# Kernel tuning notes

Hardware: AMD Instinct MI355X
Metric: run time of the kernel (lower is better)

## Reference

```python
import jax, jax.numpy as jnp
import numpy as np

NUM_HEADS = 8
NUM_LAYERS = 4
BASE_THR = 0.5     # AdaptiveLIF base_threshold (state reset -> no adaptation on single step)
TAU_MEM = 5.0      # tau_mem (single step from zero state: mem = decay*0 + x = x)
SURR_SLOPE = 5.0   # fast-sigmoid surrogate slope (forward path unaffected)
EPS = 1e-5
NEG = -1e9


@jax.custom_vjp
def spike(u):
    return (u > 0.0).astype(u.dtype)

def _spike_fwd(u):
    return (u > 0.0).astype(u.dtype), u

def _spike_bwd(u, g):
    return (g / (1.0 + SURR_SLOPE * jnp.abs(u)) ** 2,)

spike.defvjp(_spike_fwd, _spike_bwd)


def lif(x):
    # AdaptiveLIF, single timestep from reset state: mem = x, thr = base_threshold
    return spike(x - BASE_THR)


def layer_norm(x, g, b):
    m = jnp.mean(x, axis=-1, keepdims=True)
    v = jnp.mean((x - m) ** 2, axis=-1, keepdims=True)
    return (x - m) * jax.lax.rsqrt(v + EPS) * g + b


def dsa(x, wq, bq, wk, bk, wv, bv, wo, bo, top_k):
    # Dynamic Sparse Attention: dense scores -> per-query top-k mask -> softmax -> AV
    B, T, D = x.shape
    H = NUM_HEADS
    dh = D // H

    def heads(w, bias):
        return (x @ w.T + bias).reshape(B, T, H, dh).transpose(0, 2, 1, 3)  # [B,H,T,dh]

    q, k, v = heads(wq, bq), heads(wk, bk), heads(wv, bv)
    scores = jnp.einsum('bhqd,bhkd->bhqk', q, k) / jnp.sqrt(jnp.asarray(dh, x.dtype))
    vals, idx = jax.lax.top_k(scores, top_k)  # [B,H,T,K]

    # scatter top-k values into a -inf-filled score matrix (exact top-k sparsity)
    N = B * H * T
    rows = jnp.arange(N)[:, None]
    sp = jnp.full((N, T), NEG, scores.dtype).at[rows, idx.reshape(N, top_k)].set(vals.reshape(N, top_k))
    attn = jax.nn.softmax(sp.reshape(B, H, T, T), axis=-1)

    out = jnp.einsum('bhqk,bhkd->bhqd', attn, v)
    out = out.transpose(0, 2, 1, 3).reshape(B, T, D)
    out = out @ wo.T + bo
    return lif(out)  # spiking output of attention


def ffn(x, w1, b1, w2, b2):
    h = lif(x @ w1.T + b1)
    return lif(h @ w2.T + b2)


def setup_inputs() -> dict:
    key = jax.random.key(0)
    ks = jax.random.split(key, 16)
    L, D, F, IN, OUT, B, T = NUM_LAYERS, 512, 2048, 128, 256, 2, 2048
    s = 0.02
    return {
        'x': jax.random.normal(ks[0], (B, T, IN), jnp.float32),
        'emb_w': jax.random.normal(ks[1], (D, IN), jnp.float32) * s,
        'emb_b': jnp.zeros((D,), jnp.float32),
        'pos_emb': jax.random.normal(ks[2], (1, T, D), jnp.float32) * s,
        'wq': jax.random.normal(ks[3], (L, D, D), jnp.float32) * s,
        'bq': jnp.zeros((L, D), jnp.float32),
        'wk': jax.random.normal(ks[4], (L, D, D), jnp.float32) * s,
        'bk': jnp.zeros((L, D), jnp.float32),
        'wv': jax.random.normal(ks[5], (L, D, D), jnp.float32) * s,
        'bv': jnp.zeros((L, D), jnp.float32),
        'wo': jax.random.normal(ks[6], (L, D, D), jnp.float32) * s,
        'bo': jnp.zeros((L, D), jnp.float32),
        'ln1_g': jnp.ones((L, D), jnp.float32),
        'ln1_b': jnp.zeros((L, D), jnp.float32),
        'fc1_w': jax.random.normal(ks[7], (L, F, D), jnp.float32) * s,
        'fc1_b': jnp.zeros((L, F), jnp.float32),
        'fc2_w': jax.random.normal(ks[8], (L, D, F), jnp.float32) * s,
        'fc2_b': jnp.zeros((L, D), jnp.float32),
        'ln2_g': jnp.ones((L, D), jnp.float32),
        'ln2_b': jnp.zeros((L, D), jnp.float32),
        'fnorm_g': jnp.ones((D,), jnp.float32),
        'fnorm_b': jnp.zeros((D,), jnp.float32),
        'cls_w': jax.random.normal(ks[9], (OUT, D), jnp.float32) * s,
        'cls_b': jnp.zeros((OUT,), jnp.float32),
        'top_k': 32,
    }


def reference(x, emb_w, emb_b, pos_emb, wq, bq, wk, bk, wv, bv, wo, bo,
              ln1_g, ln1_b, fc1_w, fc1_b, fc2_w, fc2_b, ln2_g, ln2_b,
              fnorm_g, fnorm_b, cls_w, cls_b, top_k):
    B, T, _ = x.shape
    h = x @ emb_w.T + emb_b + pos_emb[:, :T, :]
    for l in range(NUM_LAYERS):
        a = dsa(h, wq[l], bq[l], wk[l], bk[l], wv[l], bv[l], wo[l], bo[l], top_k)
        h = layer_norm(h + a, ln1_g[l], ln1_b[l])
        f = ffn(h, fc1_w[l], fc1_b[l], fc2_w[l], fc2_b[l])
        h = layer_norm(h + f, ln2_g[l], ln2_b[l])
    h = layer_norm(h, fnorm_g, fnorm_b)
    pooled = jnp.mean(h, axis=1)  # [B, D]
    return pooled @ cls_w.T + cls_b
```

## Files before the change

kernel.cpp:

```cpp
#include <hip/hip_runtime.h>
#include <math.h>
#include <float.h>

#define T_SEQ  2048
#define DMODEL 512
#define NHEAD  8
#define DHEAD  64
#define FDIM   2048
#define NLAYER 4
#define NB     2
#define MROWS  (NB*T_SEQ)

typedef _Float16 f16x8 __attribute__((ext_vector_type(8)));
typedef float    f32x4 __attribute__((ext_vector_type(4)));

__device__ __forceinline__ void async16(const _Float16* g, _Float16* l) {
    __builtin_amdgcn_global_load_lds(
        (const __attribute__((address_space(1))) unsigned int*)g,
        (__attribute__((address_space(3))) unsigned int*)l, 16, 0, 0);
}

template<int BN, int EPI>
__global__ __launch_bounds__(256) void gemm_k(
    const float* __restrict__ A, const float* __restrict__ W,
    const float* __restrict__ bias, const float* __restrict__ pos,
    float* __restrict__ C, int M, int N, int K)
{
    constexpr int BM = 128;
    constexpr int BK = 32;
    constexpr int MN = BN / 16;
    __shared__ float As[BK][BM + 4];
    __shared__ float Ws[BK][BN + 4];
    const int tid = threadIdx.x;
    const int n0 = blockIdx.x * BN;
    const int m0 = blockIdx.y * BM;
    const int tx = tid & 15;
    const int ty = tid >> 4;

    float acc[8][MN];
    #pragma unroll
    for (int i = 0; i < 8; ++i)
        #pragma unroll
        for (int j = 0; j < MN; ++j) acc[i][j] = 0.f;

    for (int k0 = 0; k0 < K; k0 += BK) {
        #pragma unroll
        for (int it = 0; it < 4; ++it) {
            int qq = tid + 256 * it;
            int m = qq >> 3, kq = qq & 7;
            float4 v4 = *(const float4*)(A + (size_t)(m0 + m) * K + k0 + kq * 4);
            As[kq*4+0][m] = v4.x; As[kq*4+1][m] = v4.y;
            As[kq*4+2][m] = v4.z; As[kq*4+3][m] = v4.w;
        }
        #pragma unroll
        for (int it = 0; it < BN/32; ++it) {
            int qq = tid + 256 * it;
            int n = qq >> 3, kq = qq & 7;
            float4 v4 = *(const float4*)(W + (size_t)(n0 + n) * K + k0 + kq * 4);
            Ws[kq*4+0][n] = v4.x; Ws[kq*4+1][n] = v4.y;
            Ws[kq*4+2][n] = v4.z; Ws[kq*4+3][n] = v4.w;
        }
        __syncthreads();
        for (int kk = 0; kk < BK; ++kk) {
            float a[8], b[MN];
            float4 a0 = *(const float4*)&As[kk][ty*8];
            float4 a1 = *(const float4*)&As[kk][ty*8+4];
            a[0]=a0.x; a[1]=a0.y; a[2]=a0.z; a[3]=a0.w;
            a[4]=a1.x; a[5]=a1.y; a[6]=a1.z; a[7]=a1.w;
            float4 b0 = *(const float4*)&Ws[kk][tx*4];
            b[0]=b0.x; b[1]=b0.y; b[2]=b0.z; b[3]=b0.w;
            if constexpr (MN == 8) {
                float4 b1 = *(const float4*)&Ws[kk][64 + tx*4];
                b[4]=b1.x; b[5]=b1.y; b[6]=b1.z; b[7]=b1.w;
            }
            #pragma unroll
            for (int i = 0; i < 8; ++i)
                #pragma unroll
                for (int j = 0; j < MN; ++j)
                    acc[i][j] = fmaf(a[i], b[j], acc[i][j]);
        }
        __syncthreads();
    }

    #pragma unroll
    for (int i = 0; i < 8; ++i) {
        int m = m0 + ty*8 + i;
        #pragma unroll
        for (int jb = 0; jb < MN/4; ++jb) {
            int nn = n0 + jb*64 + tx*4;
            float4 r;
            r.x = acc[i][jb*4+0] + bias[nn+0];
            r.y = acc[i][jb*4+1] + bias[nn+1];
            r.z = acc[i][jb*4+2] + bias[nn+2];
            r.w = acc[i][jb*4+3] + bias[nn+3];
            if constexpr (EPI == 1) {
                const float* pp = pos + (size_t)(m & (T_SEQ-1)) * DMODEL + nn;
                r.x += pp[0]; r.y += pp[1]; r.z += pp[2]; r.w += pp[3];
            }
            *(float4*)(C + (size_t)m * N + nn) = r;
        }
    }
}

template<int BM, int ASRC, int EPI, int LAYOUT>
__global__ __launch_bounds__(256, 2) void mgemm_k(
    const _Float16* __restrict__ AH, const _Float16* __restrict__ AL,
    const _Float16* __restrict__ WH, const _Float16* __restrict__ WL,
    const float* __restrict__ bias,
    float* __restrict__ O0, float* __restrict__ O1, float* __restrict__ O2,
    float* __restrict__ O3, float* __restrict__ O4,
    int M, int N, int K)
{
    constexpr int MI = BM / 32;
    __shared__ _Float16 AsH[4][BM][8];
    __shared__ _Float16 AsL[4][BM][8];
    __shared__ _Float16 WsH[4][128][8];
    __shared__ _Float16 WsL[4][128][8];

    const int tid = threadIdx.x;
    const int n0 = blockIdx.x * 128;
    const int m0 = blockIdx.y * BM;
    const int wv = tid >> 6, lane = tid & 63;
    const int mw = (wv >> 1) * (BM/2), nw = (wv & 1) * 64;
    const int fr = lane & 15;
    const int kb = lane >> 4;

    const int wsrow = tid >> 1;
    const int wskb  = (tid & 1) * 2;
    const int wkoff = (tid & 1) * 16;

    f32x4 acc[MI][4];
    #pragma unroll
    for (int i = 0; i < MI; ++i)
        #pragma unroll
        for (int j = 0; j < 4; ++j) acc[i][j] = (f32x4)(0.f);

    for (int k0 = 0; k0 < K; k0 += 32) {
        if constexpr (BM == 128) {
            const _Float16* ap = AH + (size_t)(m0 + wsrow) * K + k0 + wkoff;
            *(f16x8*)&AsH[wskb  ][wsrow][0] = *(const f16x8*)ap;
            *(f16x8*)&AsH[wskb+1][wsrow][0] = *(const f16x8*)(ap + 8);
            if constexpr (ASRC == 0) {
                const _Float16* alp = AL + (size_t)(m0 + wsrow) * K + k0 + wkoff;
                *(f16x8*)&AsL[wskb  ][wsrow][0] = *(const f16x8*)alp;
                *(f16x8*)&AsL[wskb+1][wsrow][0] = *(const f16x8*)(alp + 8);
            }
        } else {
            const int arow = tid >> 2, akb = tid & 3;
            *(f16x8*)&AsH[akb][arow][0] =
                *(const f16x8*)(AH + (size_t)(m0 + arow) * K + k0 + akb*8);
            if constexpr (ASRC == 0)
                *(f16x8*)&AsL[akb][arow][0] =
                    *(const f16x8*)(AL + (size_t)(m0 + arow) * K + k0 + akb*8);
        }
        {
            const _Float16* wp = WH + (size_t)(n0 + wsrow) * K + k0 + wkoff;
            *(f16x8*)&WsH[wskb  ][wsrow][0] = *(const f16x8*)wp;
            *(f16x8*)&WsH[wskb+1][wsrow][0] = *(const f16x8*)(wp + 8);
            const _Float16* wlp = WL + (size_t)(n0 + wsrow) * K + k0 + wkoff;
            *(f16x8*)&WsL[wskb  ][wsrow][0] = *(const f16x8*)wlp;
            *(f16x8*)&WsL[wskb+1][wsrow][0] = *(const f16x8*)(wlp + 8);
        }
        __syncthreads();

        f16x8 aH[MI], aL[MI], bH[4], bL[4];
        #pragma unroll
        for (int i = 0; i < MI; ++i) {
            aH[i] = *(const f16x8*)&AsH[kb][mw + i*16 + fr][0];
            if constexpr (ASRC == 0) aL[i] = *(const f16x8*)&AsL[kb][mw + i*16 + fr][0];
        }
        #pragma unroll
        for (int j = 0; j < 4; ++j) {
            bH[j] = *(const f16x8*)&WsH[kb][nw + j*16 + fr][0];
            bL[j] = *(const f16x8*)&WsL[kb][nw + j*16 + fr][0];
        }
        #pragma unroll
        for (int i = 0; i < MI; ++i)
            #pragma unroll
            for (int j = 0; j < 4; ++j) {
                acc[i][j] = __builtin_amdgcn_mfma_f32_16x16x32_f16(aH[i], bH[j], acc[i][j], 0, 0, 0);
                acc[i][j] = __builtin_amdgcn_mfma_f32_16x16x32_f16(aH[i], bL[j], acc[i][j], 0, 0, 0);
                if constexpr (ASRC == 0)
                    acc[i][j] = __builtin_amdgcn_mfma_f32_16x16x32_f16(aL[i], bH[j], acc[i][j], 0, 0, 0);
            }
        __syncthreads();
    }

    const int qq = lane >> 4;
    #pragma unroll
    for (int j = 0; j < 4; ++j) {
        int n = n0 + nw + j*16 + fr;
        float bv = bias[n];
        #pragma unroll
        for (int i = 0; i < MI; ++i) {
            #pragma unroll
            for (int r = 0; r < 4; ++r) {
                int m = m0 + mw + i*16 + qq*4 + r;
                float val = acc[i][j][r] * (1.f/1024.f) + bv;
                if constexpr (EPI == 2) val = val > 0.5f ? 1.f : 0.f;
                if constexpr (EPI == 3) {
                    ((_Float16*)O0)[(size_t)m * N + n] = (val > 0.5f) ? (_Float16)16.f : (_Float16)0.f;
                } else if constexpr (LAYOUT == 0) {
                    O0[(size_t)m * N + n] = val;
                } else {
                    int b_ = m >> 11, t_ = m & (T_SEQ-1);
                    if (n < 512) {
                        size_t hl = (((size_t)(b_*NHEAD + (n>>6))*T_SEQ + t_) << 6) + (n & 63);
                        float s16 = 16.f * val;
                        _Float16 hh = (_Float16)s16;
                        ((_Float16*)O0)[hl] = hh;
                        ((_Float16*)O1)[hl] = (_Float16)(s16 - (float)hh);
                    } else if (n < 1024) {
                        int nn = n - 512;
                        size_t hl = (((size_t)(b_*NHEAD + (nn>>6))*T_SEQ + t_) << 6) + (nn & 63);
                        float s16 = 16.f * val;
                        _Float16 hh = (_Float16)s16;
                        ((_Float16*)O2)[hl] = hh;
                        ((_Float16*)O3)[hl] = (_Float16)(s16 - (float)hh);
                    } else {
                        int nn = n - 1024;
                        O4[(((size_t)(b_*NHEAD + (nn>>6))*T_SEQ + t_) << 6) + (nn & 63)] = val;
                    }
                }
            }
        }
    }
}

__global__ __launch_bounds__(256) void cvtw_k(
    const float* __restrict__ w, _Float16* __restrict__ H, _Float16* __restrict__ L,
    int n, float scale)
{
    int i = blockIdx.x * 256 + threadIdx.x;
    if (i < n) {
        float s = scale * w[i];
        _Float16 h = (_Float16)s;
        H[i] = h;
        L[i] = (_Float16)(s - (float)h);
    }
}

__global__ __launch_bounds__(256) void cvtlayer_k(
    const float* __restrict__ wq, const float* __restrict__ wk, const float* __restrict__ wv,
    const float* __restrict__ bq, const float* __restrict__ bk, const float* __restrict__ bv,
    const float* __restrict__ wo, const float* __restrict__ f1w, const float* __restrict__ f2w,
    _Float16* __restrict__ WcatH, _Float16* __restrict__ WcatL, float* __restrict__ bcat,
    _Float16* __restrict__ WoH, _Float16* __restrict__ WoL,
    _Float16* __restrict__ W1H, _Float16* __restrict__ W1L,
    _Float16* __restrict__ W2H, _Float16* __restrict__ W2L)
{
    int i = blockIdx.x * 256 + threadIdx.x;
    float w;
    _Float16 *H, *L;
    int off;
    if (i < 786432) {
        int src = i >> 18, o = i & 262143;
        w = (src == 0 ? wq : (src == 1 ? wk : wv))[o];
        H = WcatH; L = WcatL; off = i;
    } else if (i < 1048576) {
        off = i - 786432;  w = wo[off];  H = WoH; L = WoL;
    } else if (i < 2097152) {
        off = i - 1048576; w = f1w[off]; H = W1H; L = W1L;
    } else if (i < 3145728) {
        off = i - 2097152; w = f2w[off]; H = W2H; L = W2L;
    } else if (i < 3145728 + 1536) {
        int j = i - 3145728;
        int src = j >> 9, o = j & 511;
        bcat[j] = (src == 0 ? bq : (src == 1 ? bk : bv))[o];
        return;
    } else return;
    float s = 64.f * w;
    _Float16 h = (_Float16)s;
    H[off] = h;
    L[off] = (_Float16)(s - (float)h);
}

__global__ __launch_bounds__(256) void attn_k(
    const _Float16* __restrict__ qH, const _Float16* __restrict__ qL,
    const _Float16* __restrict__ kH, const _Float16* __restrict__ kL,
    const float* __restrict__ v,
    _Float16* __restrict__ outH, _Float16* __restrict__ outL)
{
    __shared__ unsigned char lds[58880];
    _Float16* ksH = (_Float16*)(lds);
    _Float16* ksL = (_Float16*)(lds + 16384);
    _Float16 (*qsH)[72] = (_Float16(*)[72])(lds + 32768);
    _Float16 (*qsL)[72] = (_Float16(*)[72])(lds + 37376);
    float    (*ss)[132] = (float(*)[132])(lds + 41984);
    float*   wrow       = (float*)(lds + 41984);
    int*     irow       = (int*)(lds + 41984 + 4224);

    const int tid = threadIdx.x;
    const int bh  = blockIdx.y;
    const int t0  = blockIdx.x * 32;
    const _Float16* qHb = qH + ((size_t)bh * T_SEQ + t0) * DHEAD;
    const _Float16* qLb = qL + ((size_t)bh * T_SEQ + t0) * DHEAD;
    const _Float16* kHb = kH + (size_t)bh * T_SEQ * DHEAD;
    const _Float16* kLb = kL + (size_t)bh * T_SEQ * DHEAD;
    const float*    vb  = v  + (size_t)bh * T_SEQ * DHEAD;

    {
        int r = tid >> 3, c = tid & 7;
        *(f16x8*)&qsH[r][c*8] = *(const f16x8*)(qHb + r*DHEAD + c*8);
        *(f16x8*)&qsL[r][c*8] = *(const f16x8*)(qLb + r*DHEAD + c*8);
    }

    unsigned kreg[32];
    #pragma unroll
    for (int i = 0; i < 32; ++i) kreg[i] = 0u;

    const int wv = tid >> 6, lane = tid & 63;
    const int fr = lane & 15, q4 = lane >> 4;
    const int c0w = wv * 32;
    const int srow = tid >> 3;
    const int ssub = tid & 7;

    auto stage = [&](int jt) {
        const int j0 = jt * 128;
        #pragma unroll
        for (int i = 0; i < 4; ++i) {
            const int r0 = wv*32 + i*8;
            const int cc = r0 + (lane >> 3);
            const int ch = (lane & 7) ^ (cc & 7);
            const size_t goff = (size_t)(j0 + cc) * DHEAD + ch*8;
            async16(kHb + goff, ksH + r0*64);
            async16(kLb + goff, ksL + r0*64);
        }
    };

    stage(0);
    __syncthreads();

    for (int jt = 0; jt < 16; ++jt) {
        const int j0 = jt * 128;

        f32x4 acc[2][2];
        acc[0][0] = (f32x4)(0.f); acc[0][1] = (f32x4)(0.f);
        acc[1][0] = (f32x4)(0.f); acc[1][1] = (f32x4)(0.f);
        #pragma unroll
        for (int ks = 0; ks < 2; ++ks) {
            const int doff = ks*32 + q4*8;
            const int chq  = ks*4 + q4;
            f16x8 aH0 = *(const f16x8*)&qsH[fr][doff];
            f16x8 aH1 = *(const f16x8*)&qsH[16 + fr][doff];
            f16x8 aL0 = *(const f16x8*)&qsL[fr][doff];
            f16x8 aL1 = *(const f16x8*)&qsL[16 + fr][doff];
            #pragma unroll
            for (int nj = 0; nj < 2; ++nj) {
                const int cc = c0w + nj*16 + fr;
                const int sl = cc*64 + (chq ^ (cc & 7))*8;
                f16x8 bHf = *(const f16x8*)&ksH[sl];
                f16x8 bLf = *(const f16x8*)&ksL[sl];
                acc[0][nj] = __builtin_amdgcn_mfma_f32_16x16x32_f16(aH0, bHf, acc[0][nj], 0, 0, 0);
                acc[0][nj] = __builtin_amdgcn_mfma_f32_16x16x32_f16(aH0, bLf, acc[0][nj], 0, 0, 0);
                acc[0][nj] = __builtin_amdgcn_mfma_f32_16x16x32_f16(aL0, bHf, acc[0][nj], 0, 0, 0);
                acc[1][nj] = __builtin_amdgcn_mfma_f32_16x16x32_f16(aH1, bHf, acc[1][nj], 0, 0, 0);
                acc[1][nj] = __builtin_amdgcn_mfma_f32_16x16x32_f16(aH1, bLf, acc[1][nj], 0, 0, 0);
                acc[1][nj] = __builtin_amdgcn_mfma_f32_16x16x32_f16(aL1, bHf, acc[1][nj], 0, 0, 0);
            }
        }
        #pragma unroll
        for (int mi = 0; mi < 2; ++mi)
            #pragma unroll
            for (int nj = 0; nj < 2; ++nj)
                #pragma unroll
                for (int r = 0; r < 4; ++r)
                    ss[mi*16 + q4*4 + r][c0w + nj*16 + fr] = acc[mi][nj][r] * (1.f/2048.f);
        __syncthreads();

        if (jt < 15) stage(jt + 1);

        float4 c4[4];
        {
            const float* ssr = &ss[srow][0] + ssub*4;
            #pragma unroll
            for (int g = 0; g < 4; ++g) c4[g] = *(const float4*)(ssr + g*32);
        }
        unsigned cand[16];
        #pragma unroll
        for (int g = 0; g < 4; ++g) {
            float vg[4] = {c4[g].x, c4[g].y, c4[g].z, c4[g].w};
            #pragma unroll
            for (int r = 0; r < 4; ++r) {
                unsigned u = __float_as_uint(vg[r]);
                u ^= (unsigned)((int)u >> 31) | 0x80000000u;
                int col = ssub*4 + g*32 + r;
                cand[g*4+r] = (u & 0xFFFFF800u) | (unsigned)(2047 - (j0 + col));
            }
        }
        #pragma unroll
        for (int k2 = 2; k2 <= 16; k2 <<= 1) {
            #pragma unroll
            for (int j2 = k2 >> 1; j2 > 0; j2 >>= 1) {
                #pragma unroll
                for (int i2 = 0; i2 < 16; ++i2) {
                    int l2 = i2 ^ j2;
                    if (l2 > i2) {
                        unsigned a = cand[i2], b = cand[l2];
                        bool sw = ((i2 & k2) == 0) ? (a < b) : (a > b);
                        cand[i2] = sw ? b : a;
                        cand[l2] = sw ? a : b;
                    }
                }
            }
        }
        #pragma unroll
        for (int j2 = 0; j2 < 16; ++j2) {
            unsigned b = cand[15 - j2];
            if (kreg[16 + j2] < b) kreg[16 + j2] = b;
        }
        #pragma unroll
        for (int st = 16; st >= 1; st >>= 1) {
            #pragma unroll
            for (int i2 = 0; i2 < 32; ++i2) {
                if ((i2 & st) == 0) {
                    unsigned lo = kreg[i2], hi = kreg[i2 | st];
                    kreg[i2]      = lo < hi ? hi : lo;
                    kreg[i2 | st] = lo < hi ? lo : hi;
                }
            }
        }
        __syncthreads();
    }

    #pragma unroll
    for (int s = 1; s <= 4; s <<= 1) {
        #pragma unroll
        for (int i = 0; i < 16; ++i) {
            unsigned pa = (unsigned)__shfl_xor((int)kreg[31-i], s, 64);
            unsigned pb = (unsigned)__shfl_xor((int)kreg[i],    s, 64);
            if (pa > kreg[i])    kreg[i]    = pa;
            if (pb > kreg[31-i]) kreg[31-i] = pb;
        }
        #pragma unroll
        for (int st = 16; st >= 1; st >>= 1) {
            #pragma unroll
            for (int i2 = 0; i2 < 32; ++i2) {
                if ((i2 & st) == 0) {
                    unsigned lo = kreg[i2], hi = kreg[i2 | st];
                    kreg[i2]      = lo < hi ? hi : lo;
                    kreg[i2 | st] = lo < hi ? lo : hi;
                }
            }
        }
    }

    if (ssub == 0) {
        float w[32];
        #pragma unroll
        for (int i = 0; i < 32; ++i) {
            unsigned um = kreg[i] & 0xFFFFF800u;
            unsigned ub = (um & 0x80000000u) ? (um ^ 0x80000000u) : ~um;
            w[i] = __uint_as_float(ub);
        }
        float m = w[0];
        float s = 0.f;
        #pragma unroll
        for (int i = 0; i < 32; ++i) { w[i] = expf(w[i] - m); s += w[i]; }
        float inv = 1.f / s;
        #pragma unroll
        for (int i = 0; i < 32; ++i) {
            wrow[srow*33 + i] = w[i] * inv;
            irow[srow*33 + i] = 2047 - (int)(kreg[i] & 0x7FFu);
        }
    }
    __syncthreads();

    const int wid = tid >> 6, lane2 = tid & 63;
    const int b = bh >> 3, h = bh & 7;
    for (int rr = wid; rr < 32; rr += 4) {
        float accv = 0.f;
        #pragma unroll
        for (int i = 0; i < 32; ++i) {
            float wgt = wrow[rr*33 + i];
            int   idx = irow[rr*33 + i];
            accv = fmaf(wgt, vb[(size_t)idx * DHEAD + lane2], accv);
        }
        size_t oi = ((size_t)(b * T_SEQ + t0 + rr)) * DMODEL + h * DHEAD + lane2;
        float s16 = 16.f * accv;
        _Float16 hh = (_Float16)s16;
        outH[oi] = hh;
        outL[oi] = (_Float16)(s16 - (float)hh);
    }
}

__global__ __launch_bounds__(256) void ln_k(
    const float* __restrict__ x, const float* __restrict__ res,
    const float* __restrict__ g, const float* __restrict__ bb,
    float* __restrict__ out, _Float16* __restrict__ oH, _Float16* __restrict__ oL)
{
    __shared__ float red[8];
    const int row = blockIdx.x;
    const int tid = threadIdx.x;
    const float* xr = x + (size_t)row * DMODEL;
    float v0 = xr[tid], v1 = xr[tid + 256];
    if (res) {
        const float* rr = res + (size_t)row * DMODEL;
        v0 += rr[tid]; v1 += rr[tid + 256];
    }
    float s = v0 + v1;
    #pragma unroll
    for (int o = 1; o < 64; o <<= 1) s += __shfl_xor(s, o);
    const int wid = tid >> 6, lane = tid & 63;
    if (lane == 0) red[wid] = s;
    __syncthreads();
    float mean = (red[0] + red[1] + red[2] + red[3]) * (1.f / DMODEL);
    float d0 = v0 - mean, d1 = v1 - mean;
    float qs = d0*d0 + d1*d1;
    #pragma unroll
    for (int o = 1; o < 64; o <<= 1) qs += __shfl_xor(qs, o);
    if (lane == 0) red[4 + wid] = qs;
    __syncthreads();
    float var = (red[4] + red[5] + red[6] + red[7]) * (1.f / DMODEL);
    float rs = rsqrtf(var + 1e-5f);
    float o0 = d0 * rs * g[tid]       + bb[tid];
    float o1 = d1 * rs * g[tid + 256] + bb[tid + 256];
    size_t base = (size_t)row * DMODEL;
    out[base + tid]       = o0;
    out[base + tid + 256] = o1;
    float s0 = 16.f * o0, s1 = 16.f * o1;
    _Float16 h0 = (_Float16)s0, h1 = (_Float16)s1;
    oH[base + tid]       = h0;
    oH[base + tid + 256] = h1;
    oL[base + tid]       = (_Float16)(s0 - (float)h0);
    oL[base + tid + 256] = (_Float16)(s1 - (float)h1);
}

__global__ __launch_bounds__(256) void pool_k(
    const float* __restrict__ h, float* __restrict__ part)
{
    const int chunk = blockIdx.x & 15;
    const int idx = (blockIdx.x >> 4) * 256 + threadIdx.x;
    const int b = idx >> 9, d = idx & 511;
    const float* p = h + ((size_t)b * T_SEQ + chunk * 128) * DMODEL + d;
    float s = 0.f;
    for (int t = 0; t < 128; ++t) s += p[(size_t)t * DMODEL];
    part[chunk * 1024 + idx] = s;
}

__global__ __launch_bounds__(256) void poolsum_k(
    const float* __restrict__ part, float* __restrict__ pooled)
{
    int idx = blockIdx.x * 256 + threadIdx.x;
    float s = 0.f;
    #pragma unroll
    for (int c = 0; c < 16; ++c) s += part[c * 1024 + idx];
    pooled[idx] = s * (1.f / T_SEQ);
}

__global__ __launch_bounds__(256) void cls_k(
    const float* __restrict__ pooled, const float* __restrict__ w,
    const float* __restrict__ bias, float* __restrict__ out)
{
    const int wid = threadIdx.x >> 6, lane = threadIdx.x & 63;
    const int oi = blockIdx.x * 4 + wid;
    const int b = oi >> 8, o = oi & 255;
    const float* pr = pooled + b * DMODEL;
    const float* wr = w + (size_t)o * DMODEL;
    float s = 0.f;
    for (int d = lane; d < DMODEL; d += 64) s = fmaf(pr[d], wr[d], s);
    #pragma unroll
    for (int off = 1; off < 64; off <<= 1) s += __shfl_xor(s, off);
    if (lane == 0) out[oi] = s + bias[o];
}

extern "C" void kernel_launch(void* const* d_in, const int* in_sizes, int n_in,
                              void* d_out, int out_size, void* d_ws, size_t ws_size,
                              hipStream_t stream)
{
    const float* x     = (const float*)d_in[0];
    const float* emb_w = (const float*)d_in[1];
    const float* emb_b = (const float*)d_in[2];
    const float* pos   = (const float*)d_in[3];
    const float* wq    = (const float*)d_in[4];
    const float* bq    = (const float*)d_in[5];
    const float* wk    = (const float*)d_in[6];
    const float* bk    = (const float*)d_in[7];
    const float* wv    = (const float*)d_in[8];
    const float* bv    = (const float*)d_in[9];
    const float* wo    = (const float*)d_in[10];
    const float* bo    = (const float*)d_in[11];
    const float* ln1g  = (const float*)d_in[12];
    const float* ln1b  = (const float*)d_in[13];
    const float* fc1w  = (const float*)d_in[14];
    const float* fc1b  = (const float*)d_in[15];
    const float* fc2w  = (const float*)d_in[16];
    const float* fc2b  = (const float*)d_in[17];
    const float* ln2g  = (const float*)d_in[18];
    const float* ln2b  = (const float*)d_in[19];
    const float* fng   = (const float*)d_in[20];
    const float* fnb   = (const float*)d_in[21];
    const float* clsw  = (const float*)d_in[22];
    const float* clsb  = (const float*)d_in[23];

    float* ws = (float*)d_ws;
    const size_t SZ  = (size_t)MROWS * DMODEL;
    const size_t HP  = SZ / 2;
    float*     h     = ws;
    float*     t1    = ws + 1*SZ;
    _Float16*  hH    = (_Float16*)(ws + 2*SZ);
    _Float16*  hL    = (_Float16*)(ws + 2*SZ + HP);
    _Float16*  aoH   = (_Float16*)(ws + 3*SZ);
    _Float16*  aoL   = (_Float16*)(ws + 3*SZ + HP);
    _Float16*  qbH   = (_Float16*)(ws + 4*SZ);
    _Float16*  qbL   = (_Float16*)(ws + 4*SZ + HP);
    _Float16*  kbH   = (_Float16*)(ws + 5*SZ);
    _Float16*  kbL   = (_Float16*)(ws + 5*SZ + HP);
    float*     vbuf  = ws + 6*SZ;
    _Float16*  WcatH = (_Float16*)(ws + 7*SZ);
    _Float16*  WcatL = (_Float16*)(ws + 7*SZ + 393216);
    _Float16*  WoH   = (_Float16*)(ws + 7*SZ + 786432);
    _Float16*  WoL   = (_Float16*)(ws + 7*SZ + 917504);
    _Float16*  W1H   = (_Float16*)(ws + 7*SZ + 1048576);
    _Float16*  W1L   = (_Float16*)(ws + 7*SZ + 1572864);
    _Float16*  W2H   = (_Float16*)(ws + 7*SZ + 2097152);
    _Float16*  W2L   = (_Float16*)(ws + 7*SZ + 2621440);
    float*     bcat  = ws + 7*SZ + 3145728;
    float*     pooled= ws + 7*SZ + 3145728 + 1536;
    float*     part  = ws + 7*SZ + 3145728 + 1536 + 1024;
    _Float16*  hid   = (_Float16*)(ws + 4*SZ);
    const size_t needed = (7*SZ + 3145728 + 1536 + 1024 + 16384) * sizeof(float);
    if (ws_size < needed) return;

    dim3 blk(256);

    gemm_k<64,1><<<dim3(DMODEL/64, MROWS/128), blk, 0, stream>>>(
        x, emb_w, emb_b, pos, h, MROWS, DMODEL, 128);
    cvtw_k<<<dim3((int)(SZ/256)), blk, 0, stream>>>(h, hH, hL, (int)SZ, 16.f);

    for (int l = 0; l < NLAYER; ++l) {
        const float* wq_l = wq + (size_t)l*DMODEL*DMODEL;
        const float* bq_l = bq + (size_t)l*DMODEL;
        const float* wk_l = wk + (size_t)l*DMODEL*DMODEL;
        const float* bk_l = bk + (size_t)l*DMODEL;
        const float* wv_l = wv + (size_t)l*DMODEL*DMODEL;
        const float* bv_l = bv + (size_t)l*DMODEL;
        const float* wo_l = wo + (size_t)l*DMODEL*DMODEL;
        const float* bo_l = bo + (size_t)l*DMODEL;
        const float* f1w_l = fc1w + (size_t)l*FDIM*DMODEL;
        const float* f1b_l = fc1b + (size_t)l*FDIM;
        const float* f2w_l = fc2w + (size_t)l*DMODEL*FDIM;
        const float* f2b_l = fc2b + (size_t)l*DMODEL;

        cvtlayer_k<<<dim3(12294), blk, 0, stream>>>(
            wq_l, wk_l, wv_l, bq_l, bk_l, bv_l, wo_l, f1w_l, f2w_l,
            WcatH, WcatL, bcat, WoH, WoL, W1H, W1L, W2H, W2L);

        mgemm_k<64,0,0,2><<<dim3(12, 64), blk, 0, stream>>>(
            hH, hL, WcatH, WcatL, bcat,
            (float*)qbH, (float*)qbL, (float*)kbH, (float*)kbL, vbuf,
            MROWS, 1536, DMODEL);

        attn_k<<<dim3(T_SEQ/32, NB*NHEAD), blk, 0, stream>>>(
            qbH, qbL, kbH, kbL, vbuf, aoH, aoL);

        mgemm_k<64,0,2,0><<<dim3(4, 64), blk, 0, stream>>>(
            aoH, aoL, WoH, WoL, bo_l, t1, nullptr, nullptr, nullptr, nullptr,
            MROWS, DMODEL, DMODEL);
        ln_k<<<dim3(MROWS), blk, 0, stream>>>(h, t1, ln1g + (size_t)l*DMODEL,
                                              ln1b + (size_t)l*DMODEL, h, hH, hL);

        mgemm_k<128,0,3,0><<<dim3(16, 32), blk, 0, stream>>>(
            hH, hL, W1H, W1L, f1b_l, (float*)hid, nullptr, nullptr, nullptr, nullptr,
            MROWS, FDIM, DMODEL);
        mgemm_k<64,1,2,0><<<dim3(4, 64), blk, 0, stream>>>(
            hid, nullptr, W2H, W2L, f2b_l, t1, nullptr, nullptr, nullptr, nullptr,
            MROWS, DMODEL, FDIM);
        ln_k<<<dim3(MROWS), blk, 0, stream>>>(h, t1, ln2g + (size_t)l*DMODEL,
                                              ln2b + (size_t)l*DMODEL, h, hH, hL);
    }

    ln_k<<<dim3(MROWS), blk, 0, stream>>>(h, nullptr, fng, fnb, h, hH, hL);
    pool_k<<<dim3(64), blk, 0, stream>>>(h, part);
    poolsum_k<<<dim3(4), blk, 0, stream>>>(part, pooled);
    cls_k<<<dim3(128), blk, 0, stream>>>(pooled, clsw, clsb, (float*)d_out);
}
```

Baseline: 1.223 ms.

## Use direct-to-LDS async loads in GEMM, keep Q in registers in attention

The split-fp16 GEMM now stages A and W tiles with global_load_lds async copies instead of loading through registers and storing to LDS. The attention kernel keeps the query fragments in registers instead of LDS, which shrinks the LDS footprint and may allow higher occupancy. The sparse AV gather also uses four independent accumulators to shorten the dependent FMA chain. The async copies change the LDS tile layout and thread-to-row mapping, and any lack of an explicit vmcnt wait before the barrier would be a correctness risk.

After: 1.338 ms. +9.4%, slower.

```diff
diff --git a/kernel.cpp b/kernel.cpp
--- a/kernel.cpp
+++ b/kernel.cpp
@@ -125,10 +125,6 @@
     const int fr = lane & 15;
     const int kb = lane >> 4;
 
-    const int wsrow = tid >> 1;
-    const int wskb  = (tid & 1) * 2;
-    const int wkoff = (tid & 1) * 16;
-
     f32x4 acc[MI][4];
     #pragma unroll
     for (int i = 0; i < MI; ++i)
@@ -137,30 +133,21 @@
 
     for (int k0 = 0; k0 < K; k0 += 32) {
         if constexpr (BM == 128) {
-            const _Float16* ap = AH + (size_t)(m0 + wsrow) * K + k0 + wkoff;
-            *(f16x8*)&AsH[wskb  ][wsrow][0] = *(const f16x8*)ap;
-            *(f16x8*)&AsH[wskb+1][wsrow][0] = *(const f16x8*)(ap + 8);
+            async16(AH + (size_t)(m0 + lane) * K + k0 + wv*8,      &AsH[wv][0][0]);
+            async16(AH + (size_t)(m0 + 64 + lane) * K + k0 + wv*8, &AsH[wv][64][0]);
             if constexpr (ASRC == 0) {
-                const _Float16* alp = AL + (size_t)(m0 + wsrow) * K + k0 + wkoff;
-                *(f16x8*)&AsL[wskb  ][wsrow][0] = *(const f16x8*)alp;
-                *(f16x8*)&AsL[wskb+1][wsrow][0] = *(const f16x8*)(alp + 8);
+                async16(AL + (size_t)(m0 + lane) * K + k0 + wv*8,      &AsL[wv][0][0]);
+                async16(AL + (size_t)(m0 + 64 + lane) * K + k0 + wv*8, &AsL[wv][64][0]);
             }
         } else {
-            const int arow = tid >> 2, akb = tid & 3;
-            *(f16x8*)&AsH[akb][arow][0] =
-                *(const f16x8*)(AH + (size_t)(m0 + arow) * K + k0 + akb*8);
+            async16(AH + (size_t)(m0 + lane) * K + k0 + wv*8, &AsH[wv][0][0]);
             if constexpr (ASRC == 0)
-                *(f16x8*)&AsL[akb][arow][0] =
-                    *(const f16x8*)(AL + (size_t)(m0 + arow) * K + k0 + akb*8);
-        }
-        {
-            const _Float16* wp = WH + (size_t)(n0 + wsrow) * K + k0 + wkoff;
-            *(f16x8*)&WsH[wskb  ][wsrow][0] = *(const f16x8*)wp;
-            *(f16x8*)&WsH[wskb+1][wsrow][0] = *(const f16x8*)(wp + 8);
-            const _Float16* wlp = WL + (size_t)(n0 + wsrow) * K + k0 + wkoff;
-            *(f16x8*)&WsL[wskb  ][wsrow][0] = *(const f16x8*)wlp;
-            *(f16x8*)&WsL[wskb+1][wsrow][0] = *(const f16x8*)(wlp + 8);
-        }
+                async16(AL + (size_t)(m0 + lane) * K + k0 + wv*8, &AsL[wv][0][0]);
+        }
+        async16(WH + (size_t)(n0 + lane) * K + k0 + wv*8,      &WsH[wv][0][0]);
+        async16(WH + (size_t)(n0 + 64 + lane) * K + k0 + wv*8, &WsH[wv][64][0]);
+        async16(WL + (size_t)(n0 + lane) * K + k0 + wv*8,      &WsL[wv][0][0]);
+        async16(WL + (size_t)(n0 + 64 + lane) * K + k0 + wv*8, &WsL[wv][64][0]);
         __syncthreads();
 
         f16x8 aH[MI], aL[MI], bH[4], bL[4];
@@ -281,14 +268,12 @@
     const float* __restrict__ v,
     _Float16* __restrict__ outH, _Float16* __restrict__ outL)
 {
-    __shared__ unsigned char lds[58880];
+    __shared__ unsigned char lds[49664];
     _Float16* ksH = (_Float16*)(lds);
     _Float16* ksL = (_Float16*)(lds + 16384);
-    _Float16 (*qsH)[72] = (_Float16(*)[72])(lds + 32768);
-    _Float16 (*qsL)[72] = (_Float16(*)[72])(lds + 37376);
-    float    (*ss)[132] = (float(*)[132])(lds + 41984);
-    float*   wrow       = (float*)(lds + 41984);
-    int*     irow       = (int*)(lds + 41984 + 4224);
+    float    (*ss)[132] = (float(*)[132])(lds + 32768);
+    float*   wrow       = (float*)(lds + 32768);
+    int*     irow       = (int*)(lds + 32768 + 4224);
 
     const int tid = threadIdx.x;
     const int bh  = blockIdx.y;
@@ -299,12 +284,6 @@
     const _Float16* kLb = kL + (size_t)bh * T_SEQ * DHEAD;
     const float*    vb  = v  + (size_t)bh * T_SEQ * DHEAD;
 
-    {
-        int r = tid >> 3, c = tid & 7;
-        *(f16x8*)&qsH[r][c*8] = *(const f16x8*)(qHb + r*DHEAD + c*8);
-        *(f16x8*)&qsL[r][c*8] = *(const f16x8*)(qLb + r*DHEAD + c*8);
-    }
-
     unsigned kreg[32];
     #pragma unroll
     for (int i = 0; i < 32; ++i) kreg[i] = 0u;
@@ -314,6 +293,16 @@
     const int c0w = wv * 32;
     const int srow = tid >> 3;
     const int ssub = tid & 7;
+
+    f16x8 qaH[2][2], qaL[2][2];
+    #pragma unroll
+    for (int ks = 0; ks < 2; ++ks) {
+        const int doff = ks*32 + q4*8;
+        qaH[ks][0] = *(const f16x8*)(qHb + fr*DHEAD + doff);
+        qaH[ks][1] = *(const f16x8*)(qHb + (16+fr)*DHEAD + doff);
+        qaL[ks][0] = *(const f16x8*)(qLb + fr*DHEAD + doff);
+        qaL[ks][1] = *(const f16x8*)(qLb + (16+fr)*DHEAD + doff);
+    }
 
     auto stage = [&](int jt) {
         const int j0 = jt * 128;
@@ -339,24 +328,19 @@
         acc[1][0] = (f32x4)(0.f); acc[1][1] = (f32x4)(0.f);
         #pragma unroll
         for (int ks = 0; ks < 2; ++ks) {
-            const int doff = ks*32 + q4*8;
             const int chq  = ks*4 + q4;
-            f16x8 aH0 = *(const f16x8*)&qsH[fr][doff];
-            f16x8 aH1 = *(const f16x8*)&qsH[16 + fr][doff];
-            f16x8 aL0 = *(const f16x8*)&qsL[fr][doff];
-            f16x8 aL1 = *(const f16x8*)&qsL[16 + fr][doff];
             #pragma unroll
             for (int nj = 0; nj < 2; ++nj) {
                 const int cc = c0w + nj*16 + fr;
                 const int sl = cc*64 + (chq ^ (cc & 7))*8;
                 f16x8 bHf = *(const f16x8*)&ksH[sl];
                 f16x8 bLf = *(const f16x8*)&ksL[sl];
-                acc[0][nj] = __builtin_amdgcn_mfma_f32_16x16x32_f16(aH0, bHf, acc[0][nj], 0, 0, 0);
-                acc[0][nj] = __builtin_amdgcn_mfma_f32_16x16x32_f16(aH0, bLf, acc[0][nj], 0, 0, 0);
-                acc[0][nj] = __builtin_amdgcn_mfma_f32_16x16x32_f16(aL0, bHf, acc[0][nj], 0, 0, 0);
-                acc[1][nj] = __builtin_amdgcn_mfma_f32_16x16x32_f16(aH1, bHf, acc[1][nj], 0, 0, 0);
-                acc[1][nj] = __builtin_amdgcn_mfma_f32_16x16x32_f16(aH1, bLf, acc[1][nj], 0, 0, 0);
-                acc[1][nj] = __builtin_amdgcn_mfma_f32_16x16x32_f16(aL1, bHf, acc[1][nj], 0, 0, 0);
+                acc[0][nj] = __builtin_amdgcn_mfma_f32_16x16x32_f16(qaH[ks][0], bHf, acc[0][nj], 0, 0, 0);
+                acc[0][nj] = __builtin_amdgcn_mfma_f32_16x16x32_f16(qaH[ks][0], bLf, acc[0][nj], 0, 0, 0);
+                acc[0][nj] = __builtin_amdgcn_mfma_f32_16x16x32_f16(qaL[ks][0], bHf, acc[0][nj], 0, 0, 0);
+                acc[1][nj] = __builtin_amdgcn_mfma_f32_16x16x32_f16(qaH[ks][1], bHf, acc[1][nj], 0, 0, 0);
+                acc[1][nj] = __builtin_amdgcn_mfma_f32_16x16x32_f16(qaH[ks][1], bLf, acc[1][nj], 0, 0, 0);
+                acc[1][nj] = __builtin_amdgcn_mfma_f32_16x16x32_f16(qaL[ks][1], bHf, acc[1][nj], 0, 0, 0);
             }
         }
         #pragma unroll
@@ -469,13 +453,15 @@
     const int wid = tid >> 6, lane2 = tid & 63;
     const int b = bh >> 3, h = bh & 7;
     for (int rr = wid; rr < 32; rr += 4) {
-        float accv = 0.f;
-        #pragma unroll
-        for (int i = 0; i < 32; ++i) {
-            float wgt = wrow[rr*33 + i];
-            int   idx = irow[rr*33 + i];
-            accv = fmaf(wgt, vb[(size_t)idx * DHEAD + lane2], accv);
-        }
+        float a0 = 0.f, a1 = 0.f, a2 = 0.f, a3 = 0.f;
+        #pragma unroll
+        for (int i = 0; i < 8; ++i) {
+            a0 = fmaf(wrow[rr*33 + i],      vb[(size_t)irow[rr*33 + i]      * DHEAD + lane2], a0);
+            a1 = fmaf(wrow[rr*33 + 8 + i],  vb[(size_t)irow[rr*33 + 8 + i]  * DHEAD + lane2], a1);
+            a2 = fmaf(wrow[rr*33 + 16 + i], vb[(size_t)irow[rr*33 + 16 + i] * DHEAD + lane2], a2);
+            a3 = fmaf(wrow[rr*33 + 24 + i], vb[(size_t)irow[rr*33 + 24 + i] * DHEAD + lane2], a3);
+        }
+        float accv = (a0 + a1) + (a2 + a3);
         size_t oi = ((size_t)(b * T_SEQ + t0 + rr)) * DMODEL + h * DHEAD + lane2;
         float s16 = 16.f * accv;
         _Float16 hh = (_Float16)s16;
```
